# Kernel tuning notes

Measured on AMD Instinct MI355X. Metric: run time of the kernel, lower is better.

Reference implementation:

```python
import jax, jax.numpy as jnp
import numpy as np

B, S, H = 8, 2048, 768      # batch, seq_len, hidden_size
N = 512                     # spans per example
MAXW = 30                   # max span width (length in [0, MAXW-1] -> width <= MAXW)


def setup_inputs() -> dict:
    key = jax.random.key(0)
    k1, k2, k3, k4 = jax.random.split(key, 4)
    embeddings = jax.random.normal(k1, (B, S, H), dtype=jnp.float32)
    starts = jax.random.randint(k2, (B, N), 0, S - MAXW)          # span starts
    lengths = jax.random.randint(k3, (B, N), 0, MAXW)             # end = start + length
    w = jax.random.normal(k4, (H, 1), dtype=jnp.float32) * 0.02   # nn.Linear(hidden, 1) weight (transposed)
    b = jnp.zeros((1,), dtype=jnp.float32)                        # linear bias
    return {"embeddings": embeddings, "w": w, "b": b, "starts": starts, "lengths": lengths}


def reference(embeddings, w, b, starts, lengths):
    # Vectorized ragged span pooling: gather up to MAXW tokens per span,
    # masked softmax over attention scores, then concat [start, end, attn].
    ends = starts + lengths                                  # inclusive end index
    offs = jnp.arange(MAXW)                                  # (W,)
    positions = starts[..., None] + offs                     # (B, N, W)
    mask = offs[None, None, :] <= lengths[..., None]         # (B, N, W) valid-token mask

    gather = jax.vmap(lambda e, p: e[p])                     # per-example gather
    span_emb = gather(embeddings, positions)                 # (B, N, W, H)

    scores = span_emb @ w + b                                # (B, N, W, 1)
    scores = jnp.where(mask[..., None], scores, -jnp.inf)
    attn_w = jax.nn.softmax(scores, axis=2)                  # masked softmax over span width
    attn_out = jnp.sum(attn_w * span_emb, axis=2)            # (B, N, H)

    start_emb = gather(embeddings, starts)                   # (B, N, H)
    end_emb = gather(embeddings, ends)                       # (B, N, H)
    return jnp.concatenate([start_emb, end_emb, attn_out], axis=-1)  # (B, N, 3H)
```

## Files before the change

kernel.cpp:

```cpp
#include <hip/hip_runtime.h>
#include <hip/hip_bf16.h>
#include <math.h>

#define BB 8
#define SS 2048
#define HH 768
#define NN 512
#define MAXW 30

__global__ __launch_bounds__(256) void sort_spans_kernel(
    const int* __restrict__ starts,
    int*       __restrict__ order)
{
    const int b   = blockIdx.x;
    const int tid = threadIdx.x;
    __shared__ int hist[SS];
    __shared__ int wsum[4];

    for (int i = tid; i < SS; i += 256) hist[i] = 0;
    __syncthreads();

    const int* st = starts + b * NN;
    for (int n = tid; n < NN; n += 256) atomicAdd(&hist[st[n]], 1);
    __syncthreads();

    const int base = tid * 8;
    int cnt[8]; int s = 0;
    #pragma unroll
    for (int k = 0; k < 8; ++k) { cnt[k] = hist[base + k]; s += cnt[k]; }

    const int lane = tid & 63, wv = tid >> 6;
    int v = s;
    #pragma unroll
    for (int off = 1; off < 64; off <<= 1) {
        int u = __shfl_up(v, off);
        if (lane >= off) v += u;
    }
    if (lane == 63) wsum[wv] = v;
    __syncthreads();
    int wbase = 0;
    #pragma unroll
    for (int k = 0; k < 4; ++k) wbase += (k < wv) ? wsum[k] : 0;

    int excl = wbase + v - s;
    #pragma unroll
    for (int k = 0; k < 8; ++k) { int c = cnt[k]; hist[base + k] = excl; excl += c; }
    __syncthreads();

    for (int n = tid; n < NN; n += 256) {
        int pos = atomicAdd(&hist[st[n]], 1);
        order[b * NN + pos] = n;
    }
}

__global__ __launch_bounds__(256) void span_fused_kernel(
    const float* __restrict__ emb,
    const float* __restrict__ w,
    const float* __restrict__ bias,
    const int*   __restrict__ starts,
    const int*   __restrict__ lengths,
    const int*   __restrict__ order,
    float*       __restrict__ out)
{
    const int tid  = threadIdx.x;
    const int wv   = tid >> 6;
    const int lane = tid & 63;
    const int bi   = blockIdx.x & 7;
    const int rank = ((int)blockIdx.x >> 3) * 4 + wv;
    const int n    = order ? order[bi * NN + rank] : rank;
    const int span = bi * NN + n;

    const int start = starts[span];
    const int len   = lengths[span];

    const float* ebase = emb + (size_t)bi * SS * HH + (size_t)start * HH;
    const int h0 = lane * 4;
    float* orow = out + (size_t)span * (3 * HH);

    const float4 w0 = *reinterpret_cast<const float4*>(w + h0);
    const float4 w1 = *reinterpret_cast<const float4*>(w + h0 + 256);
    const float4 w2 = *reinterpret_cast<const float4*>(w + h0 + 512);
    const float bb = bias[0];

    float m = -INFINITY, ssum = 0.f;
    float4 a0 = make_float4(0.f, 0.f, 0.f, 0.f), a1 = a0, a2 = a0;

    const float* row = ebase;
    float4 v0 = *reinterpret_cast<const float4*>(row + h0);
    float4 v1 = *reinterpret_cast<const float4*>(row + h0 + 256);
    float4 v2 = *reinterpret_cast<const float4*>(row + h0 + 512);

    for (int t = 0; t <= len; ++t) {
        float4 n0, n1, n2;
        if (t < len) {
            const float* nr = row + HH;
            n0 = *reinterpret_cast<const float4*>(nr + h0);
            n1 = *reinterpret_cast<const float4*>(nr + h0 + 256);
            n2 = *reinterpret_cast<const float4*>(nr + h0 + 512);
        }

        float d = v0.x * w0.x + v0.y * w0.y + v0.z * w0.z + v0.w * w0.w
                + v1.x * w1.x + v1.y * w1.y + v1.z * w1.z + v1.w * w1.w
                + v2.x * w2.x + v2.y * w2.y + v2.z * w2.z + v2.w * w2.w;
        #pragma unroll
        for (int off = 32; off; off >>= 1) d += __shfl_xor(d, off);
        d += bb;

        if (d > m) {
            const float c = __expf(m - d);
            ssum *= c;
            a0.x *= c; a0.y *= c; a0.z *= c; a0.w *= c;
            a1.x *= c; a1.y *= c; a1.z *= c; a1.w *= c;
            a2.x *= c; a2.y *= c; a2.z *= c; a2.w *= c;
            m = d;
        }
        const float pt = __expf(d - m);
        ssum += pt;
        a0.x += pt * v0.x; a0.y += pt * v0.y; a0.z += pt * v0.z; a0.w += pt * v0.w;
        a1.x += pt * v1.x; a1.y += pt * v1.y; a1.z += pt * v1.z; a1.w += pt * v1.w;
        a2.x += pt * v2.x; a2.y += pt * v2.y; a2.z += pt * v2.z; a2.w += pt * v2.w;

        if (t == 0) {
            *reinterpret_cast<float4*>(orow + h0)       = v0;
            *reinterpret_cast<float4*>(orow + h0 + 256) = v1;
            *reinterpret_cast<float4*>(orow + h0 + 512) = v2;
        }
        if (t == len) {
            *reinterpret_cast<float4*>(orow + HH + h0)       = v0;
            *reinterpret_cast<float4*>(orow + HH + h0 + 256) = v1;
            *reinterpret_cast<float4*>(orow + HH + h0 + 512) = v2;
        }

        v0 = n0; v1 = n1; v2 = n2;
        row += HH;
    }

    const float inv = 1.f / ssum;
    a0.x *= inv; a0.y *= inv; a0.z *= inv; a0.w *= inv;
    a1.x *= inv; a1.y *= inv; a1.z *= inv; a1.w *= inv;
    a2.x *= inv; a2.y *= inv; a2.z *= inv; a2.w *= inv;
    *reinterpret_cast<float4*>(orow + 2 * HH + h0)       = a0;
    *reinterpret_cast<float4*>(orow + 2 * HH + h0 + 256) = a1;
    *reinterpret_cast<float4*>(orow + 2 * HH + h0 + 512) = a2;
}

extern "C" void kernel_launch(void* const* d_in, const int* in_sizes, int n_in,
                              void* d_out, int out_size, void* d_ws, size_t ws_size,
                              hipStream_t stream) {
    const float* emb     = (const float*)d_in[0];
    const float* w       = (const float*)d_in[1];
    const float* bias    = (const float*)d_in[2];
    const int*   starts  = (const int*)d_in[3];
    const int*   lengths = (const int*)d_in[4];
    float*       out     = (float*)d_out;

    int* order = nullptr;
    if (ws_size >= (size_t)(BB * NN * sizeof(int))) {
        order = (int*)d_ws;
        sort_spans_kernel<<<dim3(BB), dim3(256), 0, stream>>>(starts, order);
    }

    span_fused_kernel<<<dim3(BB * NN / 4), dim3(256), 0, stream>>>(
        emb, w, bias, starts, lengths, order, out);
}
```

Baseline: 31.79 us.

## Precompute token scores and a bf16 copy of embeddings before span pooling

A new pre-pass reads every token once. It computes that token's attention score in fp32 and writes a bf16 copy of the embeddings plus a per-token score array into workspace. The span kernel then does a one-shot masked softmax across lanes and accumulates over the bf16 rows with a two-deep prefetch. This removes the per-span dot products and the online-softmax rescaling, and it drops the start-sorting kernel. In exchange it adds a full read and write pass over the embeddings, and the start and end outputs become bf16-rounded rather than exact copies. An fp32 fallback path is kept for when the workspace is too small.

```diff
diff --git a/kernel.cpp b/kernel.cpp
--- a/kernel.cpp
+++ b/kernel.cpp
@@ -8,58 +8,77 @@
 #define NN 512
 #define MAXW 30
 
-__global__ __launch_bounds__(256) void sort_spans_kernel(
-    const int* __restrict__ starts,
-    int*       __restrict__ order)
-{
-    const int b   = blockIdx.x;
-    const int tid = threadIdx.x;
-    __shared__ int hist[SS];
-    __shared__ int wsum[4];
-
-    for (int i = tid; i < SS; i += 256) hist[i] = 0;
-    __syncthreads();
-
-    const int* st = starts + b * NN;
-    for (int n = tid; n < NN; n += 256) atomicAdd(&hist[st[n]], 1);
-    __syncthreads();
-
-    const int base = tid * 8;
-    int cnt[8]; int s = 0;
-    #pragma unroll
-    for (int k = 0; k < 8; ++k) { cnt[k] = hist[base + k]; s += cnt[k]; }
-
-    const int lane = tid & 63, wv = tid >> 6;
-    int v = s;
-    #pragma unroll
-    for (int off = 1; off < 64; off <<= 1) {
-        int u = __shfl_up(v, off);
-        if (lane >= off) v += u;
-    }
-    if (lane == 63) wsum[wv] = v;
-    __syncthreads();
-    int wbase = 0;
-    #pragma unroll
-    for (int k = 0; k < 4; ++k) wbase += (k < wv) ? wsum[k] : 0;
-
-    int excl = wbase + v - s;
-    #pragma unroll
-    for (int k = 0; k < 8; ++k) { int c = cnt[k]; hist[base + k] = excl; excl += c; }
-    __syncthreads();
-
-    for (int n = tid; n < NN; n += 256) {
-        int pos = atomicAdd(&hist[st[n]], 1);
-        order[b * NN + pos] = n;
-    }
-}
-
-__global__ __launch_bounds__(256) void span_fused_kernel(
+static __device__ __forceinline__ unsigned short f2bf(float f) {
+    union { float f; unsigned int u; } v; v.f = f;
+    unsigned int r = (v.u + 0x7FFFu + ((v.u >> 16) & 1u)) >> 16;
+    return (unsigned short)r;
+}
+static __device__ __forceinline__ float bflo(unsigned int u) {
+    union { unsigned int u; float f; } v; v.u = u << 16; return v.f;
+}
+static __device__ __forceinline__ float bfhi(unsigned int u) {
+    union { unsigned int u; float f; } v; v.u = u & 0xFFFF0000u; return v.f;
+}
+
+__global__ __launch_bounds__(256) void conv_kernel(
     const float* __restrict__ emb,
     const float* __restrict__ w,
     const float* __restrict__ bias,
+    unsigned short* __restrict__ ebf,
+    float*       __restrict__ scores)
+{
+    const int tid  = threadIdx.x;
+    const int wv   = tid >> 6;
+    const int lane = tid & 63;
+    const int bi   = blockIdx.x & 7;
+    const int g    = (int)blockIdx.x >> 3;
+    const int t0   = g * 16 + wv * 4;
+
+    const float* eb = emb + (size_t)bi * SS * HH;
+    unsigned short* ob = ebf + (size_t)bi * SS * HH;
+
+    const int h0 = lane * 4;
+    const float4 w0 = *reinterpret_cast<const float4*>(w + h0);
+    const float4 w1 = *reinterpret_cast<const float4*>(w + h0 + 256);
+    const float4 w2 = *reinterpret_cast<const float4*>(w + h0 + 512);
+    const float bb = bias[0];
+
+    #pragma unroll
+    for (int k = 0; k < 4; ++k) {
+        const int t = t0 + k;
+        const float* rp = eb + (size_t)t * HH;
+        float4 v0 = *reinterpret_cast<const float4*>(rp + h0);
+        float4 v1 = *reinterpret_cast<const float4*>(rp + h0 + 256);
+        float4 v2 = *reinterpret_cast<const float4*>(rp + h0 + 512);
+
+        float d = v0.x * w0.x + v0.y * w0.y + v0.z * w0.z + v0.w * w0.w
+                + v1.x * w1.x + v1.y * w1.y + v1.z * w1.z + v1.w * w1.w
+                + v2.x * w2.x + v2.y * w2.y + v2.z * w2.z + v2.w * w2.w;
+        #pragma unroll
+        for (int off = 32; off; off >>= 1) d += __shfl_xor(d, off);
+
+        uint2 pa, pb, pc;
+        pa.x = (unsigned)f2bf(v0.x) | ((unsigned)f2bf(v0.y) << 16);
+        pa.y = (unsigned)f2bf(v0.z) | ((unsigned)f2bf(v0.w) << 16);
+        pb.x = (unsigned)f2bf(v1.x) | ((unsigned)f2bf(v1.y) << 16);
+        pb.y = (unsigned)f2bf(v1.z) | ((unsigned)f2bf(v1.w) << 16);
+        pc.x = (unsigned)f2bf(v2.x) | ((unsigned)f2bf(v2.y) << 16);
+        pc.y = (unsigned)f2bf(v2.z) | ((unsigned)f2bf(v2.w) << 16);
+
+        unsigned short* op = ob + (size_t)t * HH;
+        *reinterpret_cast<uint2*>(op + h0)       = pa;
+        *reinterpret_cast<uint2*>(op + h0 + 256) = pb;
+        *reinterpret_cast<uint2*>(op + h0 + 512) = pc;
+
+        if (lane == 0) scores[bi * SS + t] = d + bb;
+    }
+}
+
+__global__ __launch_bounds__(256) void span_bf16_kernel(
+    const unsigned short* __restrict__ ebf,
+    const float* __restrict__ scores,
     const int*   __restrict__ starts,
     const int*   __restrict__ lengths,
-    const int*   __restrict__ order,
     float*       __restrict__ out)
 {
     const int tid  = threadIdx.x;
@@ -67,9 +86,84 @@
     const int lane = tid & 63;
     const int bi   = blockIdx.x & 7;
     const int rank = ((int)blockIdx.x >> 3) * 4 + wv;
-    const int n    = order ? order[bi * NN + rank] : rank;
-    const int span = bi * NN + n;
-
+    const int span = bi * NN + rank;
+
+    const int start = starts[span];
+    const int len   = lengths[span];
+
+    float sc = (lane <= len) ? scores[bi * SS + start + lane] : -INFINITY;
+    float m = sc;
+    #pragma unroll
+    for (int off = 32; off; off >>= 1) m = fmaxf(m, __shfl_xor(m, off));
+    float e = (lane <= len) ? __expf(sc - m) : 0.f;
+    float sum = e;
+    #pragma unroll
+    for (int off = 32; off; off >>= 1) sum += __shfl_xor(sum, off);
+    const float p = e / sum;
+
+    const unsigned short* rb = ebf + (size_t)bi * SS * HH + (size_t)start * HH;
+    const int h0 = lane * 4;
+    float* orow = out + (size_t)span * (3 * HH);
+
+    float4 a0 = make_float4(0.f, 0.f, 0.f, 0.f), a1 = a0, a2 = a0;
+
+    const unsigned short* rp0 = rb;
+    uint2 cA = *reinterpret_cast<const uint2*>(rp0 + h0);
+    uint2 cB = *reinterpret_cast<const uint2*>(rp0 + h0 + 256);
+    uint2 cC = *reinterpret_cast<const uint2*>(rp0 + h0 + 512);
+    const unsigned short* rp1 = rb + (size_t)min(1, len) * HH;
+    uint2 xA = *reinterpret_cast<const uint2*>(rp1 + h0);
+    uint2 xB = *reinterpret_cast<const uint2*>(rp1 + h0 + 256);
+    uint2 xC = *reinterpret_cast<const uint2*>(rp1 + h0 + 512);
+
+    for (int t = 0; t <= len; ++t) {
+        const unsigned short* rp2 = rb + (size_t)min(t + 2, len) * HH;
+        uint2 yA = *reinterpret_cast<const uint2*>(rp2 + h0);
+        uint2 yB = *reinterpret_cast<const uint2*>(rp2 + h0 + 256);
+        uint2 yC = *reinterpret_cast<const uint2*>(rp2 + h0 + 512);
+
+        const float pt = __shfl(p, t);
+
+        float4 f0, f1, f2;
+        f0.x = bflo(cA.x); f0.y = bfhi(cA.x); f0.z = bflo(cA.y); f0.w = bfhi(cA.y);
+        f1.x = bflo(cB.x); f1.y = bfhi(cB.x); f1.z = bflo(cB.y); f1.w = bfhi(cB.y);
+        f2.x = bflo(cC.x); f2.y = bfhi(cC.x); f2.z = bflo(cC.y); f2.w = bfhi(cC.y);
+
+        a0.x += pt * f0.x; a0.y += pt * f0.y; a0.z += pt * f0.z; a0.w += pt * f0.w;
+        a1.x += pt * f1.x; a1.y += pt * f1.y; a1.z += pt * f1.z; a1.w += pt * f1.w;
+        a2.x += pt * f2.x; a2.y += pt * f2.y; a2.z += pt * f2.z; a2.w += pt * f2.w;
+
+        if (t == 0) {
+            *reinterpret_cast<float4*>(orow + h0)       = f0;
+            *reinterpret_cast<float4*>(orow + h0 + 256) = f1;
+            *reinterpret_cast<float4*>(orow + h0 + 512) = f2;
+        }
+        if (t == len) {
+            *reinterpret_cast<float4*>(orow + HH + h0)       = f0;
+            *reinterpret_cast<float4*>(orow + HH + h0 + 256) = f1;
+            *reinterpret_cast<float4*>(orow + HH + h0 + 512) = f2;
+        }
+
+        cA = xA; cB = xB; cC = xC;
+        xA = yA; xB = yB; xC = yC;
+    }
+
+    *reinterpret_cast<float4*>(orow + 2 * HH + h0)       = a0;
+    *reinterpret_cast<float4*>(orow + 2 * HH + h0 + 256) = a1;
+    *reinterpret_cast<float4*>(orow + 2 * HH + h0 + 512) = a2;
+}
+
+__global__ __launch_bounds__(256) void span_fused_fp32_kernel(
+    const float* __restrict__ emb, const float* __restrict__ w,
+    const float* __restrict__ bias, const int* __restrict__ starts,
+    const int* __restrict__ lengths, float* __restrict__ out)
+{
+    const int tid  = threadIdx.x;
+    const int wv   = tid >> 6;
+    const int lane = tid & 63;
+    const int bi   = blockIdx.x & 7;
+    const int rank = ((int)blockIdx.x >> 3) * 4 + wv;
+    const int span = bi * NN + rank;
     const int start = starts[span];
     const int len   = lengths[span];
 
@@ -98,14 +192,12 @@
             n1 = *reinterpret_cast<const float4*>(nr + h0 + 256);
             n2 = *reinterpret_cast<const float4*>(nr + h0 + 512);
         }
-
         float d = v0.x * w0.x + v0.y * w0.y + v0.z * w0.z + v0.w * w0.w
                 + v1.x * w1.x + v1.y * w1.y + v1.z * w1.z + v1.w * w1.w
                 + v2.x * w2.x + v2.y * w2.y + v2.z * w2.z + v2.w * w2.w;
         #pragma unroll
         for (int off = 32; off; off >>= 1) d += __shfl_xor(d, off);
         d += bb;
-
         if (d > m) {
             const float c = __expf(m - d);
             ssum *= c;
@@ -119,7 +211,6 @@
         a0.x += pt * v0.x; a0.y += pt * v0.y; a0.z += pt * v0.z; a0.w += pt * v0.w;
         a1.x += pt * v1.x; a1.y += pt * v1.y; a1.z += pt * v1.z; a1.w += pt * v1.w;
         a2.x += pt * v2.x; a2.y += pt * v2.y; a2.z += pt * v2.z; a2.w += pt * v2.w;
-
         if (t == 0) {
             *reinterpret_cast<float4*>(orow + h0)       = v0;
             *reinterpret_cast<float4*>(orow + h0 + 256) = v1;
@@ -130,11 +221,9 @@
             *reinterpret_cast<float4*>(orow + HH + h0 + 256) = v1;
             *reinterpret_cast<float4*>(orow + HH + h0 + 512) = v2;
         }
-
         v0 = n0; v1 = n1; v2 = n2;
         row += HH;
     }
-
     const float inv = 1.f / ssum;
     a0.x *= inv; a0.y *= inv; a0.z *= inv; a0.w *= inv;
     a1.x *= inv; a1.y *= inv; a1.z *= inv; a1.w *= inv;
@@ -154,12 +243,18 @@
     const int*   lengths = (const int*)d_in[4];
     float*       out     = (float*)d_out;
 
-    int* order = nullptr;
-    if (ws_size >= (size_t)(BB * NN * sizeof(int))) {
-        order = (int*)d_ws;
-        sort_spans_kernel<<<dim3(BB), dim3(256), 0, stream>>>(starts, order);
-    }
-
-    span_fused_kernel<<<dim3(BB * NN / 4), dim3(256), 0, stream>>>(
-        emb, w, bias, starts, lengths, order, out);
-}
+    const size_t ebf_bytes    = (size_t)BB * SS * HH * sizeof(unsigned short);
+    const size_t scores_bytes = (size_t)BB * SS * sizeof(float);
+
+    if (ws_size >= ebf_bytes + scores_bytes) {
+        unsigned short* ebf = (unsigned short*)d_ws;
+        float* scores = (float*)((char*)d_ws + ebf_bytes);
+
+        conv_kernel<<<dim3(1024), dim3(256), 0, stream>>>(emb, w, bias, ebf, scores);
+        span_bf16_kernel<<<dim3(BB * NN / 4), dim3(256), 0, stream>>>(
+            ebf, scores, starts, lengths, out);
+    } else {
+        span_fused_fp32_kernel<<<dim3(BB * NN / 4), dim3(256), 0, stream>>>(
+            emb, w, bias, starts, lengths, out);
+    }
+}
```

Result: no change. 32.38 us (+1.9%).
